# Optimization experiments

Hardware: AMD Instinct MI355X
Metric: run time of the kernel (lower is better)

The kernel has to match this reference:

```python
import jax, jax.numpy as jnp
import numpy as np

B, T, D = 16, 2048, 1024
TT = T - 2            # tokens after stripping BOS/EOS
WORD_EVERY = 3        # a word starts every 3 BPE tokens
MAX_WORDS = TT // WORD_EVERY  # 682
NUM_MUTEX, NUM_BIN = 64, 32


def setup_inputs() -> dict:
    key = jax.random.key(0)
    ks = jax.random.split(key, 7)
    features = jax.random.normal(ks[0], (B, T, D), dtype=jnp.float32)
    word_starts = jnp.zeros((B, TT), dtype=jnp.int32).at[:, ::WORD_EVERY].set(1)
    s = 1.0 / np.sqrt(D)
    dense_w = jax.random.normal(ks[1], (D, D), dtype=jnp.float32) * s
    dense_b = jax.random.normal(ks[2], (D,), dtype=jnp.float32) * 0.01
    out_w = jax.random.normal(ks[3], (NUM_MUTEX, D), dtype=jnp.float32) * s
    out_b = jax.random.normal(ks[4], (NUM_MUTEX,), dtype=jnp.float32) * 0.01
    bin_w = jax.random.normal(ks[5], (NUM_BIN, D + NUM_MUTEX), dtype=jnp.float32) * s
    bin_b = jax.random.normal(ks[6], (NUM_BIN,), dtype=jnp.float32) * 0.01
    return {"features": features, "word_starts": word_starts,
            "dense_w": dense_w, "dense_b": dense_b,
            "out_w": out_w, "out_b": out_b,
            "bin_w": bin_w, "bin_b": bin_b,
            "max_words": MAX_WORDS}


def _word_features(features, word_starts, max_words):
    # strip BOS/EOS
    x = features[:, 1:-1]                                  # [B, TT, D]
    b, tt, d = x.shape
    seg = jnp.cumsum(word_starts, axis=1) - 1              # word id per token; -1 before first start
    valid = seg >= 0
    flat_seg = seg + jnp.arange(b, dtype=seg.dtype)[:, None] * max_words
    overflow = b * max_words                               # dump invalid tokens into extra bucket
    flat_seg = jnp.where(valid, flat_seg, overflow).reshape(-1)
    sums = jax.ops.segment_sum(x.reshape(-1, d), flat_seg,
                               num_segments=b * max_words + 1)[:-1]
    counts = jax.ops.segment_sum(jnp.ones((b * tt,), dtype=x.dtype), flat_seg,
                                 num_segments=b * max_words + 1)[:-1]
    sums = sums.reshape(b, max_words, d)
    counts = counts.reshape(b, max_words, 1)
    # torch code initializes word_features to ONES; empty slots stay 1.0
    return jnp.where(counts > 0, sums, jnp.ones((), dtype=x.dtype))


def reference(features, word_starts, dense_w, dense_b, out_w, out_b, bin_w, bin_b, max_words):
    wf = _word_features(features, word_starts, max_words)   # [B, MW, D]
    # dropout p=0 (eval) -> identity
    h = jnp.tanh(jnp.einsum('bwd,ed->bwe', wf, dense_w) + dense_b)
    word_class_logits = jnp.einsum('bwd,cd->bwc', h, out_w) + out_b
    cat = jnp.concatenate((word_class_logits, h), axis=-1)  # [B, MW, Cm+D]
    binary_logits = jnp.einsum('bwd,cd->bwc', cat, bin_w) + bin_b
    return (word_class_logits, binary_logits)
```

## Files before the change

kernel.cpp:

```cpp
#include <hip/hip_runtime.h>
#include <stdint.h>

#define B_   16
#define T_   2048
#define D_   1024
#define TT_  2046
#define W_   682
#define BW_  (B_ * W_)
#define NMUT 64
#define NBIN 32

#define G_WF   BW_
#define G_DW   1024
#define G_OW   64
#define G_FOLD 32
#define G_ZERO 1023

typedef __attribute__((ext_vector_type(8))) short s8b;
typedef __attribute__((ext_vector_type(4))) float f32x4;

__device__ inline short f2bf(float f) {
    uint32_t u = __builtin_bit_cast(uint32_t, f);
    u += 0x7FFFu + ((u >> 16) & 1u);
    return (short)(u >> 16);
}

__device__ inline float fast_tanh(float x) {
    float xc = fminf(fmaxf(x, -15.f), 15.f);
    float e  = __expf(2.f * xc);
    return 1.f - 2.f / (e + 1.f);
}

__device__ inline void gload_lds16(const void* g, void* l) {
    __builtin_amdgcn_global_load_lds(
        (const __attribute__((address_space(1))) uint32_t*)g,
        (__attribute__((address_space(3))) uint32_t*)l, 16, 0, 0);
}

__global__ __launch_bounds__(256) void k_scan(const int* __restrict__ ws,
                                              int* __restrict__ starts,
                                              int* __restrict__ nwords) {
    __shared__ int wsum[4];
    int b = blockIdx.x;
    int tid = threadIdx.x;
    const int* row = ws + (size_t)b * TT_;
    int vals[8], incl[8];
    int p = 0;
    int t0 = tid * 8;
#pragma unroll
    for (int i = 0; i < 8; ++i) {
        int t = t0 + i;
        int v = (t < TT_) ? row[t] : 0;
        vals[i] = v;
        p += v;
        incl[i] = p;
    }
    int tot = p;
    int lane = tid & 63;
    int x = tot;
#pragma unroll
    for (int off = 1; off < 64; off <<= 1) {
        int v = __shfl_up(x, off);
        if (lane >= off) x += v;
    }
    int wid = tid >> 6;
    if (lane == 63) wsum[wid] = x;
    __syncthreads();
    int wbase = 0;
    for (int q = 0; q < wid; ++q) wbase += wsum[q];
    int excl = wbase + x - tot;
    int* st = starts + (size_t)b * (W_ + 1);
#pragma unroll
    for (int i = 0; i < 8; ++i) {
        if (vals[i]) {
            int w = excl + incl[i] - 1;
            if (w <= W_) st[w] = t0 + i;
        }
    }
    if (tid == 0) {
        int total = wsum[0] + wsum[1] + wsum[2] + wsum[3];
        nwords[b] = total < W_ ? total : W_;
        if (total <= W_) st[total] = TT_;
    }
}

__global__ __launch_bounds__(256) void k_bulk(const float* __restrict__ feat,
                                              const int* __restrict__ starts,
                                              const int* __restrict__ nwords,
                                              const float* __restrict__ dw,
                                              const float* __restrict__ ow,
                                              const float* __restrict__ ob,
                                              const float* __restrict__ bw,
                                              const float* __restrict__ bb,
                                              short* __restrict__ wf,
                                              short* __restrict__ dwb,
                                              short* __restrict__ Bcat,
                                              float* __restrict__ beff,
                                              float* __restrict__ out) {
    __shared__ float smem[NMUT];
    int blk = blockIdx.x;
    int tid = threadIdx.x;

    if (blk < G_WF) {
        int b = blk / W_;
        int w = blk - b * W_;
        short* outp = wf + (size_t)blk * D_ + tid * 4;
        int nw = nwords[b];
        f32x4 acc = (f32x4){0.f, 0.f, 0.f, 0.f};
        if (w >= nw) {
            acc = (f32x4){1.f, 1.f, 1.f, 1.f};
        } else {
            const int* st = starts + (size_t)b * (W_ + 1);
            int s = st[w], e = st[w + 1];
            const f32x4* base = (const f32x4*)(feat + ((size_t)b * T_ + 1) * D_) + tid;
            for (int t = s; t < e; ++t) {
                f32x4 v = __builtin_nontemporal_load(base + (size_t)t * (D_ / 4));
                acc += v;
            }
        }
        short4 o;
        o.x = f2bf(acc[0]); o.y = f2bf(acc[1]); o.z = f2bf(acc[2]); o.w = f2bf(acc[3]);
        *(short4*)outp = o;
    } else if (blk < G_WF + G_DW) {
        int i = (blk - G_WF) * 256 + tid;
        f32x4 v = __builtin_nontemporal_load((const f32x4*)dw + i);
        short4 o;
        o.x = f2bf(v[0]); o.y = f2bf(v[1]); o.z = f2bf(v[2]); o.w = f2bf(v[3]);
        *(short4*)(dwb + (size_t)i * 4) = o;
    } else if (blk < G_WF + G_DW + G_OW) {
        int i = (blk - (G_WF + G_DW)) * 256 + tid;
        f32x4 v = *((const f32x4*)ow + i);
        short4 o;
        o.x = f2bf(v[0]); o.y = f2bf(v[1]); o.z = f2bf(v[2]); o.w = f2bf(v[3]);
        *(short4*)(Bcat + (size_t)i * 4) = o;
    } else if (blk < G_WF + G_DW + G_OW + G_FOLD) {
        int j = blk - (G_WF + G_DW + G_OW);
        if (tid < NMUT) smem[tid] = bw[(size_t)j * (D_ + NMUT) + tid];
        __syncthreads();
        for (int k = tid; k < D_; k += 256) {
            float acc = bw[(size_t)j * (D_ + NMUT) + NMUT + k];
#pragma unroll 8
            for (int c = 0; c < NMUT; ++c)
                acc = fmaf(smem[c], ow[(size_t)c * D_ + k], acc);
            Bcat[(size_t)(NMUT + j) * D_ + k] = f2bf(acc);
        }
        if (tid == 0) {
            float acc = bb[j];
            for (int c = 0; c < NMUT; ++c) acc = fmaf(smem[c], ob[c], acc);
            beff[j] = acc;
        }
    } else {
        int i = (blk - (G_WF + G_DW + G_OW + G_FOLD)) * 1024 + tid * 4;
        *(f32x4*)(out + i) = (f32x4){0.f, 0.f, 0.f, 0.f};
    }
}

__global__ __launch_bounds__(256) void k_gemm1(const short* __restrict__ wf,
                                               const short* __restrict__ dwb,
                                               const float* __restrict__ db,
                                               const short* __restrict__ Bcat,
                                               const float* __restrict__ ob,
                                               const float* __restrict__ beff,
                                               float* __restrict__ out) {
    __shared__ short SMEM[16384];
    short* As = SMEM;
    short* Bs = SMEM + 8192;
    int tid  = threadIdx.x;
    int lane = tid & 63;
    int w    = tid >> 6;
    int wm = w >> 1, wn = w & 1;
    int bm = blockIdx.x * 128;
    int bn = blockIdx.y * 128;

    int ln = lane & 15;
    int qk = lane >> 4;

    int srow = lane >> 2;
    int scol = (lane & 3) * 8;

    f32x4 acc[4][4];
#pragma unroll
    for (int i = 0; i < 4; ++i)
#pragma unroll
        for (int j = 0; j < 4; ++j) acc[i][j] = (f32x4){0.f, 0.f, 0.f, 0.f};

    for (int kt = 0; kt < D_; kt += 64) {
#pragma unroll
        for (int hh = 0; hh < 2; ++hh) {
#pragma unroll
            for (int p = 0; p < 2; ++p) {
                int chunk = w * 2 + p;
                int arow = bm + chunk * 16 + srow;
                arow = arow < BW_ ? arow : BW_ - 1;
                gload_lds16(wf + (size_t)arow * D_ + kt + hh * 32 + scol,
                            &As[hh * 4096 + chunk * 512]);
                int brow = bn + chunk * 16 + srow;
                gload_lds16(dwb + (size_t)brow * D_ + kt + hh * 32 + scol,
                            &Bs[hh * 4096 + chunk * 512]);
            }
        }
        __syncthreads();
#pragma unroll
        for (int hh = 0; hh < 2; ++hh) {
            s8b af[4], bf[4];
#pragma unroll
            for (int i = 0; i < 4; ++i)
                af[i] = *(const s8b*)&As[hh * 4096 + (wm * 64 + i * 16 + ln) * 32 + qk * 8];
#pragma unroll
            for (int j = 0; j < 4; ++j)
                bf[j] = *(const s8b*)&Bs[hh * 4096 + (wn * 64 + j * 16 + ln) * 32 + qk * 8];
#pragma unroll
            for (int i = 0; i < 4; ++i)
#pragma unroll
                for (int j = 0; j < 4; ++j)
                    acc[i][j] = __builtin_amdgcn_mfma_f32_16x16x32_bf16(
                        af[i], bf[j], acc[i][j], 0, 0, 0);
        }
        __syncthreads();
    }

    short* Ht = SMEM;
    float bias[4];
#pragma unroll
    for (int j = 0; j < 4; ++j) bias[j] = db[bn + wn * 64 + j * 16 + ln];
#pragma unroll
    for (int i = 0; i < 4; ++i) {
#pragma unroll
        for (int j = 0; j < 4; ++j) {
            int lcol = wn * 64 + j * 16 + ln;
#pragma unroll
            for (int r = 0; r < 4; ++r) {
                int lrow = wm * 64 + i * 16 + qk * 4 + r;
                Ht[(lrow * 128 + lcol) ^ ((lrow & 7) << 3)] =
                    f2bf(fast_tanh(acc[i][j][r] + bias[j]));
            }
        }
    }
    __syncthreads();

    f32x4 accE[2][6];
#pragma unroll
    for (int i = 0; i < 2; ++i)
#pragma unroll
        for (int cj = 0; cj < 6; ++cj) accE[i][cj] = (f32x4){0.f, 0.f, 0.f, 0.f};

    const short* bp = Bcat + (size_t)ln * D_ + bn + qk * 8;
#pragma unroll
    for (int kk = 0; kk < 4; ++kk) {
        s8b af[2];
#pragma unroll
        for (int i = 0; i < 2; ++i) {
            int row = w * 32 + i * 16 + ln;
            int sc  = kk * 32 + qk * 8;
            af[i] = *(const s8b*)&Ht[(row * 128 + sc) ^ ((row & 7) << 3)];
        }
#pragma unroll
        for (int cj = 0; cj < 6; ++cj) {
            s8b bf = *(const s8b*)(bp + (size_t)cj * 16 * D_ + kk * 32);
#pragma unroll
            for (int i = 0; i < 2; ++i)
                accE[i][cj] = __builtin_amdgcn_mfma_f32_16x16x32_bf16(
                    af[i], bf, accE[i][cj], 0, 0, 0);
        }
    }

    float bj[6];
    bool addb = (blockIdx.y == 0);
#pragma unroll
    for (int cj = 0; cj < 6; ++cj) {
        int c = cj * 16 + ln;
        bj[cj] = addb ? ((c < NMUT) ? ob[c] : beff[c - NMUT]) : 0.f;
    }
#pragma unroll
    for (int i = 0; i < 2; ++i) {
#pragma unroll
        for (int r = 0; r < 4; ++r) {
            int gr = bm + w * 32 + i * 16 + qk * 4 + r;
            if (gr < BW_) {
#pragma unroll
                for (int cj = 0; cj < 6; ++cj) {
                    int c = cj * 16 + ln;
                    float v = accE[i][cj][r] + bj[cj];
                    if (c < NMUT)
                        atomicAdd(&out[(size_t)gr * NMUT + c], v);
                    else
                        atomicAdd(&out[(size_t)BW_ * NMUT + (size_t)gr * NBIN + (c - NMUT)], v);
                }
            }
        }
    }
}

extern "C" void kernel_launch(void* const* d_in, const int* in_sizes, int n_in,
                              void* d_out, int out_size, void* d_ws, size_t ws_size,
                              hipStream_t stream) {
    const float* feat    = (const float*)d_in[0];
    const int*   wstarts = (const int*)d_in[1];
    const float* dw      = (const float*)d_in[2];
    const float* db      = (const float*)d_in[3];
    const float* ow      = (const float*)d_in[4];
    const float* ob      = (const float*)d_in[5];
    const float* bw      = (const float*)d_in[6];
    const float* bb      = (const float*)d_in[7];
    float* out = (float*)d_out;

    char* ws = (char*)d_ws;
    size_t off = 0;
    auto alloc = [&](size_t bytes) {
        void* p = ws + off;
        off += (bytes + 255) & ~(size_t)255;
        return p;
    };
    short* wf     = (short*)alloc((size_t)BW_ * D_ * 2);
    short* dwb    = (short*)alloc((size_t)D_ * D_ * 2);
    short* Bcat   = (short*)alloc((size_t)(NMUT + NBIN) * D_ * 2);
    float* beff   = (float*)alloc(NBIN * 4);
    int*   starts = (int*)alloc((size_t)B_ * (W_ + 1) * 4);
    int*   nwords = (int*)alloc(B_ * 4);

    k_scan<<<16, 256, 0, stream>>>(wstarts, starts, nwords);
    k_bulk<<<G_WF + G_DW + G_OW + G_FOLD + G_ZERO, 256, 0, stream>>>(
        feat, starts, nwords, dw, ow, ob, bw, bb, wf, dwb, Bcat, beff, out);
    k_gemm1<<<dim3((BW_ + 127) / 128, D_ / 128), 256, 0, stream>>>(
        wf, dwb, db, Bcat, ob, beff, out);
}
```

Baseline: 288.6 us.

## Split fused epilogue GEMM into separate kernel, removing atomics and output zeroing

The second projection was fused into the first GEMM's epilogue, with partial sums over eight N-tiles combined via fp32 atomicAdd, and the output had to be zeroed in advance. Now the first GEMM writes tanh(h) as bf16 to a workspace buffer. A new k_gemm2 kernel then computes the 96 output columns per 16-row tile, reducing the K-split across waves in LDS and doing plain stores. This removes the atomics and the zero-fill blocks, but adds a write and read of the 22 MB h buffer and one more kernel launch.

```diff
diff --git a/kernel.cpp b/kernel.cpp
--- a/kernel.cpp
+++ b/kernel.cpp
@@ -14,7 +14,6 @@
 #define G_DW   1024
 #define G_OW   64
 #define G_FOLD 32
-#define G_ZERO 1023
 
 typedef __attribute__((ext_vector_type(8))) short s8b;
 typedef __attribute__((ext_vector_type(4))) float f32x4;
@@ -95,8 +94,7 @@
                                               short* __restrict__ wf,
                                               short* __restrict__ dwb,
                                               short* __restrict__ Bcat,
-                                              float* __restrict__ beff,
-                                              float* __restrict__ out) {
+                                              float* __restrict__ beff) {
     __shared__ float smem[NMUT];
     int blk = blockIdx.x;
     int tid = threadIdx.x;
@@ -133,7 +131,7 @@
         short4 o;
         o.x = f2bf(v[0]); o.y = f2bf(v[1]); o.z = f2bf(v[2]); o.w = f2bf(v[3]);
         *(short4*)(Bcat + (size_t)i * 4) = o;
-    } else if (blk < G_WF + G_DW + G_OW + G_FOLD) {
+    } else {
         int j = blk - (G_WF + G_DW + G_OW);
         if (tid < NMUT) smem[tid] = bw[(size_t)j * (D_ + NMUT) + tid];
         __syncthreads();
@@ -149,22 +147,15 @@
             for (int c = 0; c < NMUT; ++c) acc = fmaf(smem[c], ob[c], acc);
             beff[j] = acc;
         }
-    } else {
-        int i = (blk - (G_WF + G_DW + G_OW + G_FOLD)) * 1024 + tid * 4;
-        *(f32x4*)(out + i) = (f32x4){0.f, 0.f, 0.f, 0.f};
     }
 }
 
 __global__ __launch_bounds__(256) void k_gemm1(const short* __restrict__ wf,
                                                const short* __restrict__ dwb,
                                                const float* __restrict__ db,
-                                               const short* __restrict__ Bcat,
-                                               const float* __restrict__ ob,
-                                               const float* __restrict__ beff,
-                                               float* __restrict__ out) {
-    __shared__ short SMEM[16384];
-    short* As = SMEM;
-    short* Bs = SMEM + 8192;
+                                               short* __restrict__ h) {
+    __shared__ short As[2][128 * 32];
+    __shared__ short Bs[2][128 * 32];
     int tid  = threadIdx.x;
     int lane = tid & 63;
     int w    = tid >> 6;
@@ -193,10 +184,10 @@
                 int arow = bm + chunk * 16 + srow;
                 arow = arow < BW_ ? arow : BW_ - 1;
                 gload_lds16(wf + (size_t)arow * D_ + kt + hh * 32 + scol,
-                            &As[hh * 4096 + chunk * 512]);
+                            &As[hh][chunk * 512]);
                 int brow = bn + chunk * 16 + srow;
                 gload_lds16(dwb + (size_t)brow * D_ + kt + hh * 32 + scol,
-                            &Bs[hh * 4096 + chunk * 512]);
+                            &Bs[hh][chunk * 512]);
             }
         }
         __syncthreads();
@@ -205,10 +196,10 @@
             s8b af[4], bf[4];
 #pragma unroll
             for (int i = 0; i < 4; ++i)
-                af[i] = *(const s8b*)&As[hh * 4096 + (wm * 64 + i * 16 + ln) * 32 + qk * 8];
+                af[i] = *(const s8b*)&As[hh][(wm * 64 + i * 16 + ln) * 32 + qk * 8];
 #pragma unroll
             for (int j = 0; j < 4; ++j)
-                bf[j] = *(const s8b*)&Bs[hh * 4096 + (wn * 64 + j * 16 + ln) * 32 + qk * 8];
+                bf[j] = *(const s8b*)&Bs[hh][(wn * 64 + j * 16 + ln) * 32 + qk * 8];
 #pragma unroll
             for (int i = 0; i < 4; ++i)
 #pragma unroll
@@ -219,75 +210,72 @@
         __syncthreads();
     }
 
-    short* Ht = SMEM;
     float bias[4];
 #pragma unroll
     for (int j = 0; j < 4; ++j) bias[j] = db[bn + wn * 64 + j * 16 + ln];
 #pragma unroll
     for (int i = 0; i < 4; ++i) {
-#pragma unroll
-        for (int j = 0; j < 4; ++j) {
-            int lcol = wn * 64 + j * 16 + ln;
-#pragma unroll
-            for (int r = 0; r < 4; ++r) {
-                int lrow = wm * 64 + i * 16 + qk * 4 + r;
-                Ht[(lrow * 128 + lcol) ^ ((lrow & 7) << 3)] =
-                    f2bf(fast_tanh(acc[i][j][r] + bias[j]));
+        int row0 = bm + wm * 64 + i * 16 + qk * 4;
+#pragma unroll
+        for (int r = 0; r < 4; ++r) {
+            int row = row0 + r;
+            if (row < BW_) {
+#pragma unroll
+                for (int j = 0; j < 4; ++j) {
+                    int cn = bn + wn * 64 + j * 16 + ln;
+                    h[(size_t)row * D_ + cn] =
+                        f2bf(fast_tanh(acc[i][j][r] + bias[j]));
+                }
             }
         }
     }
-    __syncthreads();
-
-    f32x4 accE[2][6];
-#pragma unroll
-    for (int i = 0; i < 2; ++i)
-#pragma unroll
-        for (int cj = 0; cj < 6; ++cj) accE[i][cj] = (f32x4){0.f, 0.f, 0.f, 0.f};
-
-    const short* bp = Bcat + (size_t)ln * D_ + bn + qk * 8;
-#pragma unroll
-    for (int kk = 0; kk < 4; ++kk) {
-        s8b af[2];
-#pragma unroll
-        for (int i = 0; i < 2; ++i) {
-            int row = w * 32 + i * 16 + ln;
-            int sc  = kk * 32 + qk * 8;
-            af[i] = *(const s8b*)&Ht[(row * 128 + sc) ^ ((row & 7) << 3)];
-        }
+}
+
+__global__ __launch_bounds__(256) void k_gemm2(const short* __restrict__ h,
+                                               const short* __restrict__ Bcat,
+                                               const float* __restrict__ ob,
+                                               const float* __restrict__ beff,
+                                               float* __restrict__ out) {
+    __shared__ float red[4][6][256];
+    int tid  = threadIdx.x;
+    int lane = tid & 63;
+    int w    = tid >> 6;
+    int ln = lane & 15, qk = lane >> 4;
+    int m0 = blockIdx.x * 16;
+
+    const short* ap = h    + (size_t)(m0 + ln) * D_ + w * 256 + qk * 8;
+    const short* bp = Bcat + (size_t)ln        * D_ + w * 256 + qk * 8;
+
+    f32x4 acc[6];
+#pragma unroll
+    for (int cj = 0; cj < 6; ++cj) acc[cj] = (f32x4){0.f, 0.f, 0.f, 0.f};
+
+#pragma unroll
+    for (int kk = 0; kk < 8; ++kk) {
+        s8b af = *(const s8b*)(ap + kk * 32);
 #pragma unroll
         for (int cj = 0; cj < 6; ++cj) {
             s8b bf = *(const s8b*)(bp + (size_t)cj * 16 * D_ + kk * 32);
-#pragma unroll
-            for (int i = 0; i < 2; ++i)
-                accE[i][cj] = __builtin_amdgcn_mfma_f32_16x16x32_bf16(
-                    af[i], bf, accE[i][cj], 0, 0, 0);
-        }
-    }
-
-    float bj[6];
-    bool addb = (blockIdx.y == 0);
-#pragma unroll
-    for (int cj = 0; cj < 6; ++cj) {
-        int c = cj * 16 + ln;
-        bj[cj] = addb ? ((c < NMUT) ? ob[c] : beff[c - NMUT]) : 0.f;
-    }
-#pragma unroll
-    for (int i = 0; i < 2; ++i) {
-#pragma unroll
-        for (int r = 0; r < 4; ++r) {
-            int gr = bm + w * 32 + i * 16 + qk * 4 + r;
-            if (gr < BW_) {
-#pragma unroll
-                for (int cj = 0; cj < 6; ++cj) {
-                    int c = cj * 16 + ln;
-                    float v = accE[i][cj][r] + bj[cj];
-                    if (c < NMUT)
-                        atomicAdd(&out[(size_t)gr * NMUT + c], v);
-                    else
-                        atomicAdd(&out[(size_t)BW_ * NMUT + (size_t)gr * NBIN + (c - NMUT)], v);
-                }
-            }
-        }
+            acc[cj] = __builtin_amdgcn_mfma_f32_16x16x32_bf16(af, bf, acc[cj], 0, 0, 0);
+        }
+    }
+
+#pragma unroll
+    for (int cj = 0; cj < 6; ++cj)
+        *(f32x4*)&red[w][cj][lane * 4] = acc[cj];
+    __syncthreads();
+
+#pragma unroll
+    for (int i = tid; i < 1536; i += 256) {
+        int cj = i >> 8;
+        int e  = i & 255;
+        float v = red[0][cj][e] + red[1][cj][e] + red[2][cj][e] + red[3][cj][e];
+        int l = e >> 2, r = e & 3;
+        int row = m0 + (l >> 4) * 4 + r;
+        int c   = cj * 16 + (l & 15);
+        v += (c < NMUT) ? ob[c] : beff[c - NMUT];
+        if (c < NMUT) out[(size_t)row * NMUT + c] = v;
+        else out[(size_t)BW_ * NMUT + (size_t)row * NBIN + (c - NMUT)] = v;
     }
 }
 
@@ -312,6 +300,7 @@
         return p;
     };
     short* wf     = (short*)alloc((size_t)BW_ * D_ * 2);
+    short* h      = (short*)alloc((size_t)BW_ * D_ * 2);
     short* dwb    = (short*)alloc((size_t)D_ * D_ * 2);
     short* Bcat   = (short*)alloc((size_t)(NMUT + NBIN) * D_ * 2);
     float* beff   = (float*)alloc(NBIN * 4);
@@ -319,8 +308,8 @@
     int*   nwords = (int*)alloc(B_ * 4);
 
     k_scan<<<16, 256, 0, stream>>>(wstarts, starts, nwords);
-    k_bulk<<<G_WF + G_DW + G_OW + G_FOLD + G_ZERO, 256, 0, stream>>>(
-        feat, starts, nwords, dw, ow, ob, bw, bb, wf, dwb, Bcat, beff, out);
-    k_gemm1<<<dim3((BW_ + 127) / 128, D_ / 128), 256, 0, stream>>>(
-        wf, dwb, db, Bcat, ob, beff, out);
-}
+    k_bulk<<<G_WF + G_DW + G_OW + G_FOLD, 256, 0, stream>>>(
+        feat, starts, nwords, dw, ow, ob, bw, bb, wf, dwb, Bcat, beff);
+    k_gemm1<<<dim3((BW_ + 127) / 128, D_ / 128), 256, 0, stream>>>(wf, dwb, db, h);
+    k_gemm2<<<BW_ / 16, 256, 0, stream>>>(h, Bcat, ob, beff, out);
+}
```

New measurement: 270.9 us. 1.07x faster.
